# Kernel tuning notes

Measured on AMD Instinct MI355X. Metric: run time of the kernel, lower is better.

The kernel has to match this reference:

```python
import jax, jax.numpy as jnp
import numpy as np

MARGIN = 1.0
EPS = 1e-6
DIAG_BIG = 99999.0


def setup_inputs() -> dict:
    key = jax.random.key(0)
    x = jax.random.normal(key, (16384, 256), dtype=jnp.float32)
    # HardNet descriptors are unit-L2 normalized (the distance formula assumes it)
    x = x / jnp.linalg.norm(x, axis=1, keepdims=True)
    return {"x": x}


def reference(x) -> jnp.ndarray:
    cnt = x.shape[0] // 2
    a = x[:cnt]          # [N, d] anchors
    p = x[cnt:]          # [N, d] positives
    # pairwise unit-L2 distance: sqrt((1 - a.p^T + eps) * 2)
    dmat = jnp.sqrt((1.0 - jnp.matmul(a, p.T) + EPS) * 2.0)  # [N, N]
    pos = jnp.diagonal(dmat)                                  # [N]
    # mask diagonal with large constant, then row/col mins = hard negatives
    masked = dmat + jnp.eye(cnt, dtype=dmat.dtype) * DIAG_BIG
    min_a = jnp.min(masked, axis=0)   # best negative anchor per positive
    min_p = jnp.min(masked, axis=1)   # best negative positive per anchor
    neg = jnp.minimum(min_a, min_p)   # [N]
    return jnp.mean(jnp.clip(MARGIN - neg + pos, 0.0))
```

## Files before the change

kernel.cpp:

```cpp
#include <hip/hip_runtime.h>
#include <hip/hip_fp8.h>


#define CNT   8192
#define KDIM  256
#define BIGF  3.0e38f

typedef float f32x4 __attribute__((ext_vector_type(4)));

__device__ __forceinline__ unsigned short f2bf(float f) {
    unsigned u = __float_as_uint(f);
    u += 0x7FFFu + ((u >> 16) & 1u);
    return (unsigned short)(u >> 16);
}

__device__ __forceinline__ unsigned cvt4_fp8(float a, float b, float c, float d) {
#if __has_builtin(__builtin_amdgcn_cvt_pk_fp8_f32)
    unsigned v = __builtin_amdgcn_cvt_pk_fp8_f32(a, b, 0, false);
    v = __builtin_amdgcn_cvt_pk_fp8_f32(c, d, v, true);
    return v;
#else
    return (unsigned)__hip_fp8_e4m3(a).__x |
           ((unsigned)__hip_fp8_e4m3(b).__x << 8) |
           ((unsigned)__hip_fp8_e4m3(c).__x << 16) |
           ((unsigned)__hip_fp8_e4m3(d).__x << 24);
#endif
}

__device__ __forceinline__ long mk64(unsigned lo, unsigned hi) {
    return (long)(((unsigned long long)hi << 32) | (unsigned long long)lo);
}


__global__ __launch_bounds__(256) void convert8_kernel(
    const float* __restrict__ x, unsigned char* __restrict__ xb,
    unsigned* __restrict__ mins)
{
    int T    = blockIdx.x * 256 + threadIdx.x;
    int lane = T & 63;
    int ks2  = (T >> 6) & 3;
    int rg   = T >> 8;
    int quad = lane >> 4;
    int m    = lane & 15;
    int row  = rg * 16 + m;
    const float* src = x + (size_t)row * 256 + ks2 * 64 + quad * 8;
    float4 u0 = *(const float4*)(src);
    float4 u1 = *(const float4*)(src + 4);
    float4 u2 = *(const float4*)(src + 32);
    float4 u3 = *(const float4*)(src + 36);
    uint4 w;
    w.x = cvt4_fp8(u0.x, u0.y, u0.z, u0.w);
    w.y = cvt4_fp8(u1.x, u1.y, u1.z, u1.w);
    w.z = cvt4_fp8(u2.x, u2.y, u2.z, u2.w);
    w.w = cvt4_fp8(u3.x, u3.y, u3.z, u3.w);
    *(uint4*)(xb + (size_t)T * 16) = w;
    if (T < 2 * CNT) mins[T] = 0x7F7FFFFFu;
}

#define TST 132
__global__ __launch_bounds__(256, 2) void dist6_kernel(
    const unsigned char* __restrict__ Ab, const unsigned char* __restrict__ Pb,
    unsigned* __restrict__ g_rowmin, unsigned* __restrict__ g_colmin,
    float* __restrict__ g_pos)
{
    __shared__ float T[32 * TST];

    const int tid  = threadIdx.x;
    const int l    = blockIdx.x;
    const int xcd  = l & 7;
    const int i    = l >> 3;
    const int bm   = (xcd >> 1) * 16 + (i & 15);
    const int bn   = (xcd & 1) * 16 + (i >> 4);

    const int wave = tid >> 6;
    const int lane = tid & 63;
    const int quad = lane >> 4;
    const int l15  = lane & 15;
    const int wm   = wave >> 1;
    const int wn   = wave & 1;

    f32x4 acc[4][8];
    #pragma unroll
    for (int a = 0; a < 4; a++)
        #pragma unroll
        for (int b = 0; b < 8; b++)
            acc[a][b] = (f32x4){0.f, 0.f, 0.f, 0.f};

    const char* Abase = (const char*)Ab + lane * 16;
    const char* Pbase = (const char*)Pb + lane * 16;
    size_t a_off[4], b_off[8];
    #pragma unroll
    for (int mi = 0; mi < 4; mi++)
        a_off[mi] = ((size_t)(bm * 8 + wm * 4 + mi) << 12);
    #pragma unroll
    for (int ni = 0; ni < 8; ni++)
        b_off[ni] = ((size_t)(bn * 16 + wn * 8 + ni) << 12);

    #pragma unroll
    for (int ks2 = 0; ks2 < 4; ks2++) {
        uint4 a4[4], b4[8];
        #pragma unroll
        for (int mi = 0; mi < 4; mi++)
            a4[mi] = *(const uint4*)(Abase + a_off[mi] + ks2 * 1024);
        #pragma unroll
        for (int ni = 0; ni < 8; ni++)
            b4[ni] = *(const uint4*)(Pbase + b_off[ni] + ks2 * 1024);
        #pragma unroll
        for (int h = 0; h < 2; h++) {
            long af[4], bf[8];
            #pragma unroll
            for (int mi = 0; mi < 4; mi++)
                af[mi] = h ? mk64(a4[mi].z, a4[mi].w) : mk64(a4[mi].x, a4[mi].y);
            #pragma unroll
            for (int ni = 0; ni < 8; ni++)
                bf[ni] = h ? mk64(b4[ni].z, b4[ni].w) : mk64(b4[ni].x, b4[ni].y);
            #pragma unroll
            for (int mi = 0; mi < 4; mi++)
                #pragma unroll
                for (int ni = 0; ni < 8; ni++)
                    acc[mi][ni] = __builtin_amdgcn_mfma_f32_16x16x32_fp8_fp8(
                        af[mi], bf[ni], acc[mi][ni], 0, 0, 0);
        }
    }


    if ((bm >> 1) == bn) {
        const int dstart = (bm & 1) * 128;
        #pragma unroll
        for (int mi = 0; mi < 4; mi++)
            #pragma unroll
            for (int ni = 0; ni < 8; ni++)
                #pragma unroll
                for (int r = 0; r < 4; r++) {
                    int rl = wm * 64 + mi * 16 + quad * 4 + r;
                    int cl = wn * 128 + ni * 16 + l15;
                    if (cl == rl + dstart) {
                        g_pos[bm * 128 + rl] = (1.0f - acc[mi][ni][r] + 1e-6f) * 2.0f;
                        acc[mi][ni][r] = -BIGF;
                    }
                }
    }

    #pragma unroll
    for (int ni = 0; ni < 8; ni++) {
        float v = -BIGF;
        #pragma unroll
        for (int mi = 0; mi < 4; mi++)
            #pragma unroll
            for (int r = 0; r < 4; r++)
                v = fmaxf(v, acc[mi][ni][r]);
        v = fmaxf(v, __shfl_xor(v, 16, 64));
        v = fmaxf(v, __shfl_xor(v, 32, 64));
        if (quad == 0) {
            float tt = fmaxf((1.0f - v + 1e-6f) * 2.0f, 0.0f);
            atomicMin(&g_colmin[bn * 256 + wn * 128 + ni * 16 + l15],
                      __float_as_uint(tt));
        }
    }

    float rmax[4][4];
    #pragma unroll
    for (int mi = 0; mi < 4; mi++)
        #pragma unroll
        for (int r = 0; r < 4; r++) {
            float v = acc[mi][0][r];
            #pragma unroll
            for (int ni = 1; ni < 8; ni++) v = fmaxf(v, acc[mi][ni][r]);
            rmax[mi][r] = v;
        }
    const int centry = wn * 16 + l15;
    #pragma unroll
    for (int mi = 0; mi < 4; mi++) {
        f32x4 v = {rmax[mi][0], rmax[mi][1], rmax[mi][2], rmax[mi][3]};
        *(f32x4*)&T[centry * TST + wm * 64 + mi * 16 + quad * 4] = v;
    }
    __syncthreads();

    if (tid < 128) {
        int row = tid;
        float v0 = T[row], v1 = T[TST + row];
        #pragma unroll
        for (int c = 2; c < 32; c += 2) {
            v0 = fmaxf(v0, T[c * TST + row]);
            v1 = fmaxf(v1, T[(c + 1) * TST + row]);
        }
        float v = fmaxf(v0, v1);
        float tt = fmaxf((1.0f - v + 1e-6f) * 2.0f, 0.0f);
        atomicMin(&g_rowmin[bm * 128 + row], __float_as_uint(tt));
    }
}

__global__ __launch_bounds__(1024) void finalize_t_kernel(
    const unsigned* __restrict__ rm, const unsigned* __restrict__ cm,
    const float* __restrict__ post, float* __restrict__ out)
{
    float local = 0.f;
    for (int i = threadIdx.x; i < CNT; i += 1024) {
        float t   = fminf(__uint_as_float(rm[i]), __uint_as_float(cm[i]));
        float neg = sqrtf(fmaxf(t, 0.f));
        float pos = sqrtf(fmaxf(post[i], 0.f));
        local += fmaxf(1.0f - neg + pos, 0.0f);
    }
    #pragma unroll
    for (int m = 1; m < 64; m <<= 1) local += __shfl_xor(local, m, 64);
    __shared__ float wsum[16];
    if ((threadIdx.x & 63) == 0) wsum[threadIdx.x >> 6] = local;
    __syncthreads();
    if (threadIdx.x == 0) {
        float s = 0.f;
        #pragma unroll
        for (int w = 0; w < 16; w++) s += wsum[w];
        out[0] = s * (1.0f / (float)CNT);
    }
}


#define BM 128
#define BN 128
#define BK 64
#define KST (BK + 8)

typedef __bf16 bf16x8 __attribute__((ext_vector_type(8)));

__global__ __launch_bounds__(256) void init_min_kernel(unsigned* buf, int n) {
    int i = blockIdx.x * 256 + threadIdx.x;
    if (i < n) buf[i] = 0x7F7FFFFFu;
}

__global__ __launch_bounds__(256) void dist_tile_kernel(
    const float* __restrict__ A, const float* __restrict__ P,
    unsigned* __restrict__ g_rowmin, unsigned* __restrict__ g_colmin,
    float* __restrict__ g_pos)
{
    __shared__ unsigned short As[BM * KST];
    __shared__ unsigned short Bs[BN * KST];
    __shared__ unsigned redrow[BM];
    __shared__ unsigned redcol[BN];

    const int tid  = threadIdx.x;
    const int bm   = blockIdx.y;
    const int bn   = blockIdx.x;
    const int wave = tid >> 6;
    const int lane = tid & 63;
    const int quad = lane >> 4;
    const int l15  = lane & 15;
    const int m_off = (wave >> 1) * 64;
    const int n_off = (wave & 1) * 64;

    if (tid < BM) redrow[tid] = 0x7F7FFFFFu;
    if (tid < BN) redcol[tid] = 0x7F7FFFFFu;

    f32x4 acc[4][4];
    #pragma unroll
    for (int i = 0; i < 4; i++)
        #pragma unroll
        for (int j = 0; j < 4; j++)
            acc[i][j] = (f32x4){0.f, 0.f, 0.f, 0.f};

    const int srow = tid >> 4;
    const int scol = tid & 15;

    for (int kc = 0; kc < KDIM / BK; kc++) {
        #pragma unroll
        for (int i = 0; i < 8; i++) {
            int r = srow + i * 16;
            float4 va = *(const float4*)(A + (size_t)(bm * BM + r) * KDIM + kc * BK + scol * 4);
            float4 vb = *(const float4*)(P + (size_t)(bn * BN + r) * KDIM + kc * BK + scol * 4);
            ushort4 wa, wb;
            wa.x = f2bf(va.x); wa.y = f2bf(va.y); wa.z = f2bf(va.z); wa.w = f2bf(va.w);
            wb.x = f2bf(vb.x); wb.y = f2bf(vb.y); wb.z = f2bf(vb.z); wb.w = f2bf(vb.w);
            *(ushort4*)(&As[r * KST + scol * 4]) = wa;
            *(ushort4*)(&Bs[r * KST + scol * 4]) = wb;
        }
        __syncthreads();
        #pragma unroll
        for (int ks = 0; ks < BK / 32; ks++) {
            bf16x8 af[4], bfr[4];
            #pragma unroll
            for (int mi = 0; mi < 4; mi++)
                af[mi] = *(const bf16x8*)(&As[(m_off + mi * 16 + l15) * KST + ks * 32 + quad * 8]);
            #pragma unroll
            for (int ni = 0; ni < 4; ni++)
                bfr[ni] = *(const bf16x8*)(&Bs[(n_off + ni * 16 + l15) * KST + ks * 32 + quad * 8]);
            #pragma unroll
            for (int mi = 0; mi < 4; mi++)
                #pragma unroll
                for (int ni = 0; ni < 4; ni++)
                    acc[mi][ni] = __builtin_amdgcn_mfma_f32_16x16x32_bf16(
                        af[mi], bfr[ni], acc[mi][ni], 0, 0, 0);
        }
        __syncthreads();
    }

    float rmin[4][4], cmin[4];
    #pragma unroll
    for (int mi = 0; mi < 4; mi++)
        #pragma unroll
        for (int r = 0; r < 4; r++) rmin[mi][r] = BIGF;
    #pragma unroll
    for (int ni = 0; ni < 4; ni++) cmin[ni] = BIGF;

    const int grow0 = bm * BM + m_off + quad * 4;
    const int gcol0 = bn * BN + n_off + l15;

    #pragma unroll
    for (int mi = 0; mi < 4; mi++)
        #pragma unroll
        for (int ni = 0; ni < 4; ni++) {
            int gcol = gcol0 + ni * 16;
            #pragma unroll
            for (int r = 0; r < 4; r++) {
                int grow = grow0 + mi * 16 + r;
                float s = acc[mi][ni][r];
                float d = sqrtf((1.0f - s + 1e-6f) * 2.0f);
                float dm = d;
                if (grow == gcol) { g_pos[grow] = d; dm = BIGF; }
                rmin[mi][r] = fminf(rmin[mi][r], dm);
                cmin[ni]    = fminf(cmin[ni], dm);
            }
        }

    #pragma unroll
    for (int mi = 0; mi < 4; mi++)
        #pragma unroll
        for (int r = 0; r < 4; r++) {
            float v = rmin[mi][r];
            v = fminf(v, __shfl_xor(v, 1, 64));
            v = fminf(v, __shfl_xor(v, 2, 64));
            v = fminf(v, __shfl_xor(v, 4, 64));
            v = fminf(v, __shfl_xor(v, 8, 64));
            rmin[mi][r] = v;
        }
    #pragma unroll
    for (int ni = 0; ni < 4; ni++) {
        float v = cmin[ni];
        v = fminf(v, __shfl_xor(v, 16, 64));
        v = fminf(v, __shfl_xor(v, 32, 64));
        cmin[ni] = v;
    }

    if (l15 == 0) {
        #pragma unroll
        for (int mi = 0; mi < 4; mi++)
            #pragma unroll
            for (int r = 0; r < 4; r++)
                atomicMin(&redrow[m_off + mi * 16 + quad * 4 + r],
                          __float_as_uint(rmin[mi][r]));
    }
    if (quad == 0) {
        #pragma unroll
        for (int ni = 0; ni < 4; ni++)
            atomicMin(&redcol[n_off + ni * 16 + l15], __float_as_uint(cmin[ni]));
    }
    __syncthreads();

    if (tid < 128) atomicMin(&g_rowmin[bm * BM + tid], redrow[tid]);
    else           atomicMin(&g_colmin[bn * BN + (tid - 128)], redcol[tid - 128]);
}

__global__ __launch_bounds__(1024) void finalize_kernel(
    const unsigned* __restrict__ g_rowmin, const unsigned* __restrict__ g_colmin,
    const float* __restrict__ g_pos, float* __restrict__ out)
{
    float local = 0.f;
    for (int i = threadIdx.x; i < CNT; i += 1024) {
        float neg = fminf(__uint_as_float(g_rowmin[i]), __uint_as_float(g_colmin[i]));
        float v = 1.0f - neg + g_pos[i];
        local += fmaxf(v, 0.0f);
    }
    #pragma unroll
    for (int m = 1; m < 64; m <<= 1) local += __shfl_xor(local, m, 64);
    __shared__ float wsum[16];
    if ((threadIdx.x & 63) == 0) wsum[threadIdx.x >> 6] = local;
    __syncthreads();
    if (threadIdx.x == 0) {
        float s = 0.f;
        #pragma unroll
        for (int w = 0; w < 16; w++) s += wsum[w];
        out[0] = s * (1.0f / (float)CNT);
    }
}


extern "C" void kernel_launch(void* const* d_in, const int* in_sizes, int n_in,
                              void* d_out, int out_size, void* d_ws, size_t ws_size,
                              hipStream_t stream) {
    const float* x = (const float*)d_in[0];
    float* out = (float*)d_out;

    const size_t fp8_bytes = (size_t)2 * CNT * KDIM;
    const size_t need = fp8_bytes + (size_t)2 * CNT * 4 + (size_t)CNT * 4;

    if (ws_size >= need) {
        unsigned char* xb   = (unsigned char*)d_ws;
        unsigned*      mins = (unsigned*)((char*)d_ws + fp8_bytes);
        float*         pos  = (float*)(mins + 2 * CNT);
        convert8_kernel<<<dim3(1024), dim3(256), 0, stream>>>(x, xb, mins);
        dist6_kernel<<<dim3(2048), dim3(256), 0, stream>>>(
            xb, xb + (size_t)CNT * KDIM, mins, mins + CNT, pos);
        finalize_t_kernel<<<dim3(1), dim3(1024), 0, stream>>>(mins, mins + CNT, pos, out);
    } else {
        unsigned* rowmin = (unsigned*)d_ws;
        unsigned* colmin = rowmin + CNT;
        float*    pos    = (float*)(colmin + CNT);
        init_min_kernel<<<dim3(2 * CNT / 256), dim3(256), 0, stream>>>(rowmin, 2 * CNT);
        dist_tile_kernel<<<dim3(CNT / BN, CNT / BM), dim3(256), 0, stream>>>(
            x, x + (size_t)CNT * KDIM, rowmin, colmin, pos);
        finalize_kernel<<<dim3(1), dim3(1024), 0, stream>>>(rowmin, colmin, pos, out);
    }
}
```

Before: 102.4 us.

## Switch FP8 distance GEMM to 32x32x64 scaled MFMA with matching fragment layout

Replaces the 16x16x32 FP8 MFMA tiling with the gfx950 mfma_scale 32x32x64 f8f6f4 instruction using unit scales, so each wave issues fewer, larger matrix ops per K step. The convert kernel now writes fp8 fragments in the 32-row/64-K layout that instruction expects, and the diagonal, column-min and row-min epilogues are remapped to the 32x32 accumulator register layout, with a larger shared transpose buffer. The aim is higher MFMA throughput and fewer instruction issues. The cost is a more involved register-to-row mapping in the epilogue and twice the shared memory for the row reduction.

```diff
diff --git a/kernel.cpp b/kernel.cpp
--- a/kernel.cpp
+++ b/kernel.cpp
@@ -2,11 +2,16 @@
 #include <hip/hip_fp8.h>
 
 
-#define CNT   8192
-#define KDIM  256
-#define BIGF  3.0e38f
-
-typedef float f32x4 __attribute__((ext_vector_type(4)));
+#define CNT    8192
+#define KDIM   256
+#define BIGF   3.0e38f
+#define SCALE1 0x7F7F7F7F
+
+typedef float f32x4  __attribute__((ext_vector_type(4)));
+typedef float f32x16 __attribute__((ext_vector_type(16)));
+typedef int   v8i    __attribute__((ext_vector_type(8)));
+
+union frag8 { uint4 q[2]; v8i v; };
 
 __device__ __forceinline__ unsigned short f2bf(float f) {
     unsigned u = __float_as_uint(f);
@@ -27,27 +32,24 @@
 #endif
 }
 
-__device__ __forceinline__ long mk64(unsigned lo, unsigned hi) {
-    return (long)(((unsigned long long)hi << 32) | (unsigned long long)lo);
-}
-
-
-__global__ __launch_bounds__(256) void convert8_kernel(
+
+__global__ __launch_bounds__(256) void convert_mx_kernel(
     const float* __restrict__ x, unsigned char* __restrict__ xb,
     unsigned* __restrict__ mins)
 {
     int T    = blockIdx.x * 256 + threadIdx.x;
     int lane = T & 63;
-    int ks2  = (T >> 6) & 3;
-    int rg   = T >> 8;
-    int quad = lane >> 4;
-    int m    = lane & 15;
-    int row  = rg * 16 + m;
-    const float* src = x + (size_t)row * 256 + ks2 * 64 + quad * 8;
+    int h    = (T >> 6) & 1;
+    int c    = T >> 7;
+    int kc64 = c & 3;
+    int rg   = c >> 2;
+    int row  = rg * 32 + (lane & 31);
+    int col0 = kc64 * 64 + (lane >> 5) * 32 + h * 16;
+    const float* src = x + (size_t)row * KDIM + col0;
     float4 u0 = *(const float4*)(src);
     float4 u1 = *(const float4*)(src + 4);
-    float4 u2 = *(const float4*)(src + 32);
-    float4 u3 = *(const float4*)(src + 36);
+    float4 u2 = *(const float4*)(src + 8);
+    float4 u3 = *(const float4*)(src + 12);
     uint4 w;
     w.x = cvt4_fp8(u0.x, u0.y, u0.z, u0.w);
     w.y = cvt4_fp8(u1.x, u1.y, u1.z, u1.w);
@@ -57,13 +59,13 @@
     if (T < 2 * CNT) mins[T] = 0x7F7FFFFFu;
 }
 
-#define TST 132
-__global__ __launch_bounds__(256, 2) void dist6_kernel(
+#define TST 136
+__global__ __launch_bounds__(256, 2) void dist7_kernel(
     const unsigned char* __restrict__ Ab, const unsigned char* __restrict__ Pb,
     unsigned* __restrict__ g_rowmin, unsigned* __restrict__ g_colmin,
     float* __restrict__ g_pos)
 {
-    __shared__ float T[32 * TST];
+    __shared__ float T[64 * TST];
 
     const int tid  = threadIdx.x;
     const int l    = blockIdx.x;
@@ -74,115 +76,113 @@
 
     const int wave = tid >> 6;
     const int lane = tid & 63;
-    const int quad = lane >> 4;
-    const int l15  = lane & 15;
+    const int l31  = lane & 31;
+    const int kh   = lane >> 5;
     const int wm   = wave >> 1;
     const int wn   = wave & 1;
 
-    f32x4 acc[4][8];
-    #pragma unroll
-    for (int a = 0; a < 4; a++)
-        #pragma unroll
-        for (int b = 0; b < 8; b++)
-            acc[a][b] = (f32x4){0.f, 0.f, 0.f, 0.f};
+    f32x16 acc[2][4];
+    #pragma unroll
+    for (int a = 0; a < 2; a++)
+        #pragma unroll
+        for (int b = 0; b < 4; b++)
+            #pragma unroll
+            for (int r = 0; r < 16; r++)
+                acc[a][b][r] = 0.f;
 
     const char* Abase = (const char*)Ab + lane * 16;
     const char* Pbase = (const char*)Pb + lane * 16;
-    size_t a_off[4], b_off[8];
-    #pragma unroll
-    for (int mi = 0; mi < 4; mi++)
-        a_off[mi] = ((size_t)(bm * 8 + wm * 4 + mi) << 12);
-    #pragma unroll
-    for (int ni = 0; ni < 8; ni++)
-        b_off[ni] = ((size_t)(bn * 16 + wn * 8 + ni) << 12);
-
-    #pragma unroll
-    for (int ks2 = 0; ks2 < 4; ks2++) {
-        uint4 a4[4], b4[8];
-        #pragma unroll
-        for (int mi = 0; mi < 4; mi++)
-            a4[mi] = *(const uint4*)(Abase + a_off[mi] + ks2 * 1024);
-        #pragma unroll
-        for (int ni = 0; ni < 8; ni++)
-            b4[ni] = *(const uint4*)(Pbase + b_off[ni] + ks2 * 1024);
-        #pragma unroll
-        for (int h = 0; h < 2; h++) {
-            long af[4], bf[8];
-            #pragma unroll
-            for (int mi = 0; mi < 4; mi++)
-                af[mi] = h ? mk64(a4[mi].z, a4[mi].w) : mk64(a4[mi].x, a4[mi].y);
-            #pragma unroll
-            for (int ni = 0; ni < 8; ni++)
-                bf[ni] = h ? mk64(b4[ni].z, b4[ni].w) : mk64(b4[ni].x, b4[ni].y);
-            #pragma unroll
-            for (int mi = 0; mi < 4; mi++)
-                #pragma unroll
-                for (int ni = 0; ni < 8; ni++)
-                    acc[mi][ni] = __builtin_amdgcn_mfma_f32_16x16x32_fp8_fp8(
-                        af[mi], bf[ni], acc[mi][ni], 0, 0, 0);
-        }
+    size_t a_off[2], b_off[4];
+    #pragma unroll
+    for (int mi = 0; mi < 2; mi++)
+        a_off[mi] = (size_t)(bm * 4 + wm * 2 + mi) << 13;
+    #pragma unroll
+    for (int ni = 0; ni < 4; ni++)
+        b_off[ni] = (size_t)(bn * 8 + wn * 4 + ni) << 13;
+
+    #pragma unroll
+    for (int kc = 0; kc < 4; kc++) {
+        frag8 af[2], bf[4];
+        #pragma unroll
+        for (int mi = 0; mi < 2; mi++) {
+            af[mi].q[0] = *(const uint4*)(Abase + a_off[mi] + kc * 2048);
+            af[mi].q[1] = *(const uint4*)(Abase + a_off[mi] + kc * 2048 + 1024);
+        }
+        #pragma unroll
+        for (int ni = 0; ni < 4; ni++) {
+            bf[ni].q[0] = *(const uint4*)(Pbase + b_off[ni] + kc * 2048);
+            bf[ni].q[1] = *(const uint4*)(Pbase + b_off[ni] + kc * 2048 + 1024);
+        }
+        #pragma unroll
+        for (int mi = 0; mi < 2; mi++)
+            #pragma unroll
+            for (int ni = 0; ni < 4; ni++)
+                acc[mi][ni] = __builtin_amdgcn_mfma_scale_f32_32x32x64_f8f6f4(
+                    af[mi].v, bf[ni].v, acc[mi][ni],
+                    0, 0,
+                    0, SCALE1,
+                    0, SCALE1);
     }
 
 
     if ((bm >> 1) == bn) {
         const int dstart = (bm & 1) * 128;
         #pragma unroll
-        for (int mi = 0; mi < 4; mi++)
-            #pragma unroll
-            for (int ni = 0; ni < 8; ni++)
+        for (int mi = 0; mi < 2; mi++)
+            #pragma unroll
+            for (int ni = 0; ni < 4; ni++)
                 #pragma unroll
-                for (int r = 0; r < 4; r++) {
-                    int rl = wm * 64 + mi * 16 + quad * 4 + r;
-                    int cl = wn * 128 + ni * 16 + l15;
+                for (int reg = 0; reg < 16; reg++) {
+                    int rl = wm * 64 + mi * 32 + (reg & 3) + 8 * (reg >> 2) + 4 * kh;
+                    int cl = wn * 128 + ni * 32 + l31;
                     if (cl == rl + dstart) {
-                        g_pos[bm * 128 + rl] = (1.0f - acc[mi][ni][r] + 1e-6f) * 2.0f;
-                        acc[mi][ni][r] = -BIGF;
+                        g_pos[bm * 128 + rl] = (1.0f - acc[mi][ni][reg] + 1e-6f) * 2.0f;
+                        acc[mi][ni][reg] = -BIGF;
                     }
                 }
     }
 
     #pragma unroll
-    for (int ni = 0; ni < 8; ni++) {
+    for (int ni = 0; ni < 4; ni++) {
         float v = -BIGF;
         #pragma unroll
-        for (int mi = 0; mi < 4; mi++)
-            #pragma unroll
-            for (int r = 0; r < 4; r++)
-                v = fmaxf(v, acc[mi][ni][r]);
-        v = fmaxf(v, __shfl_xor(v, 16, 64));
+        for (int mi = 0; mi < 2; mi++)
+            #pragma unroll
+            for (int reg = 0; reg < 16; reg++)
+                v = fmaxf(v, acc[mi][ni][reg]);
         v = fmaxf(v, __shfl_xor(v, 32, 64));
-        if (quad == 0) {
+        if (kh == 0) {
             float tt = fmaxf((1.0f - v + 1e-6f) * 2.0f, 0.0f);
-            atomicMin(&g_colmin[bn * 256 + wn * 128 + ni * 16 + l15],
+            atomicMin(&g_colmin[bn * 256 + wn * 128 + ni * 32 + l31],
                       __float_as_uint(tt));
         }
     }
 
-    float rmax[4][4];
-    #pragma unroll
-    for (int mi = 0; mi < 4; mi++)
-        #pragma unroll
-        for (int r = 0; r < 4; r++) {
-            float v = acc[mi][0][r];
-            #pragma unroll
-            for (int ni = 1; ni < 8; ni++) v = fmaxf(v, acc[mi][ni][r]);
-            rmax[mi][r] = v;
-        }
-    const int centry = wn * 16 + l15;
-    #pragma unroll
-    for (int mi = 0; mi < 4; mi++) {
-        f32x4 v = {rmax[mi][0], rmax[mi][1], rmax[mi][2], rmax[mi][3]};
-        *(f32x4*)&T[centry * TST + wm * 64 + mi * 16 + quad * 4] = v;
-    }
+    const int entry = wn * 32 + l31;
+    #pragma unroll
+    for (int mi = 0; mi < 2; mi++)
+        #pragma unroll
+        for (int q = 0; q < 4; q++) {
+            f32x4 v;
+            #pragma unroll
+            for (int rr = 0; rr < 4; rr++) {
+                float m = acc[mi][0][q * 4 + rr];
+                #pragma unroll
+                for (int ni = 1; ni < 4; ni++)
+                    m = fmaxf(m, acc[mi][ni][q * 4 + rr]);
+                v[rr] = m;
+            }
+            *(f32x4*)&T[entry * TST + wm * 64 + mi * 32 + q * 8 + kh * 4] = v;
+        }
     __syncthreads();
 
     if (tid < 128) {
         int row = tid;
         float v0 = T[row], v1 = T[TST + row];
         #pragma unroll
-        for (int c = 2; c < 32; c += 2) {
-            v0 = fmaxf(v0, T[c * TST + row]);
-            v1 = fmaxf(v1, T[(c + 1) * TST + row]);
+        for (int e = 2; e < 64; e += 2) {
+            v0 = fmaxf(v0, T[e * TST + row]);
+            v1 = fmaxf(v1, T[(e + 1) * TST + row]);
         }
         float v = fmaxf(v0, v1);
         float tt = fmaxf((1.0f - v + 1e-6f) * 2.0f, 0.0f);
@@ -395,8 +395,8 @@
         unsigned char* xb   = (unsigned char*)d_ws;
         unsigned*      mins = (unsigned*)((char*)d_ws + fp8_bytes);
         float*         pos  = (float*)(mins + 2 * CNT);
-        convert8_kernel<<<dim3(1024), dim3(256), 0, stream>>>(x, xb, mins);
-        dist6_kernel<<<dim3(2048), dim3(256), 0, stream>>>(
+        convert_mx_kernel<<<dim3(1024), dim3(256), 0, stream>>>(x, xb, mins);
+        dist7_kernel<<<dim3(2048), dim3(256), 0, stream>>>(
             xb, xb + (size_t)CNT * KDIM, mins, mins + CNT, pos);
         finalize_t_kernel<<<dim3(1), dim3(1024), 0, stream>>>(mins, mins + CNT, pos, out);
     } else {
```

Result: faster. 93.01 us (-9.1%).
